# Optimization experiments

Hardware: AMD Instinct MI355X
Metric: run time of the kernel (lower is better)

Reference implementation:

```python
import jax, jax.numpy as jnp
import numpy as np

NUM_KEYPOINTS = 2048
SAMPLE_RADIUS = 1.6
NUM_SECTORS = 6
NEG = jnp.float32(-1e10)
POS = jnp.float32(1e10)


def setup_inputs() -> dict:
    key = jax.random.key(0)
    kxy, kz, kc, kcz, kd, ky = jax.random.split(key, 6)
    B, N, M = 2, 65536, 128
    pts_xy = jax.random.uniform(kxy, (B, N, 2), minval=-70.0, maxval=70.0)
    pts_z = jax.random.uniform(kz, (B, N, 1), minval=-3.0, maxval=1.0)
    points = jnp.concatenate([pts_xy, pts_z], axis=-1)  # [B,N,3]
    ctr_xy = jax.random.uniform(kc, (B, M, 2), minval=-60.0, maxval=60.0)
    ctr_z = jax.random.uniform(kcz, (B, M, 1), minval=-2.0, maxval=0.0)
    dims = jax.random.uniform(kd, (B, M, 3), minval=1.0, maxval=4.5)
    yaw = jax.random.uniform(ky, (B, M, 1), minval=-np.pi, maxval=np.pi)
    rois = jnp.concatenate([ctr_xy, ctr_z, dims, yaw], axis=-1)  # [B,M,7]
    return {"points": points, "rois": rois}


def _masked_fps(xyz, mask, K):
    """Farthest point sampling restricted to mask; returns K indices into xyz.
    Matches mmcv furthest_point_sample: squared distances, start at first point."""
    first = jnp.argmax(mask)  # first valid point in original order
    dmin = jnp.where(mask, POS, NEG)

    def step(carry, _):
        dmin, last = carry
        d = jnp.sum((xyz - xyz[last]) ** 2, axis=-1)
        dmin = jnp.minimum(dmin, jnp.where(mask, d, NEG))
        nxt = jnp.argmax(dmin)
        return (dmin, nxt), nxt

    (_, _), rest = jax.lax.scan(step, (dmin, first), None, length=K - 1)
    return jnp.concatenate([first[None], rest])  # [K]


def _spc_single(points, rois):
    """points: [N,3] float, rois: [M,7]. Returns [NUM_KEYPOINTS,3]."""
    N = points.shape[0]
    K = NUM_KEYPOINTS
    # geometric center: z += dz/2 (done in forward before sampling)
    rois = rois.at[:, 2].add(rois[:, 5] * 0.5)
    # --- sample_points_with_roi: point-to-ROI-center distance filter ---
    diff = points[:, None, :] - rois[None, :, 0:3]          # [N,M,3]
    dist = jnp.linalg.norm(diff, axis=-1)                   # [N,M]
    min_dis = jnp.min(dist, axis=-1)
    min_idx = jnp.argmin(dist, axis=-1)
    roi_max_dim = jnp.linalg.norm(rois[min_idx, 3:6] * 0.5, axis=-1)
    valid = min_dis < roi_max_dim + SAMPLE_RADIUS           # [N]
    total = jnp.maximum(jnp.sum(valid), 1)
    # --- sector_fps ---
    sector_size = 2.0 * np.pi / NUM_SECTORS
    angles = jnp.arctan2(points[:, 1], points[:, 0]) + np.pi
    sector = jnp.clip(jnp.floor(angles / sector_size), 0, NUM_SECTORS).astype(jnp.int32)
    masks = valid[None, :] & (sector[None, :] == jnp.arange(NUM_SECTORS)[:, None])  # [S,N]
    cnt = jnp.sum(masks, axis=-1)                           # [S]
    # per-sector budget: min(cnt_k, ceil(cnt_k / total * K)), 0 for empty sectors
    n_k = jnp.minimum(cnt, jnp.ceil(cnt.astype(jnp.float32) * K / total).astype(cnt.dtype))
    fps_idx = jax.vmap(_masked_fps, in_axes=(None, 0, None))(points, masks, K)  # [S,K]
    # concatenate the first n_k picks of each sector in sector order
    offsets = jnp.concatenate([jnp.zeros((1,), n_k.dtype), jnp.cumsum(n_k)[:-1]])
    pos = offsets[:, None] + jnp.arange(K)[None, :]          # [S,K] slot in concat order
    keep = jnp.arange(K)[None, :] < n_k[:, None]
    pos = jnp.where(keep, pos, K)                            # out-of-range -> dropped
    buf = jnp.zeros((K,), jnp.int32)
    buf = buf.at[pos.reshape(-1)].set(fps_idx.reshape(-1).astype(jnp.int32), mode='drop')
    # truncate / cyclic-repeat to exactly K keypoints
    s_total = jnp.maximum(jnp.sum(n_k), 1)
    out_idx = buf[jnp.arange(K) % s_total]
    return points[out_idx]                                   # [K,3]


def reference(points, rois):
    return jax.vmap(_spc_single)(points, rois)  # [B,K,3]
```

## Files before the change

### kernel.cpp

```cpp
#include <hip/hip_runtime.h>
#include <cmath>
#include <cstdint>

#pragma clang fp contract(off)

#define B_ 2
#define N_ 65536
#define M_ 128
#define K_ 2048
#define S_ 6
#define NBLK 256
#define CT 256
#define FPS_T 512
#define NW 8
#define RMAX 8
#define CAP (FPS_T * RMAX)

#define PI_F 3.14159265358979323846f
#define SS_F 1.0471975511965976f

__device__ __forceinline__ unsigned long long wave_max_u64_dpp(unsigned long long key) {
#define DPP_STEP(CTRL)                                                          \
    {                                                                           \
        unsigned lo = (unsigned)key, hi = (unsigned)(key >> 32);                \
        unsigned olo = (unsigned)__builtin_amdgcn_update_dpp(0, (int)lo, CTRL, 0xf, 0xf, true); \
        unsigned ohi = (unsigned)__builtin_amdgcn_update_dpp(0, (int)hi, CTRL, 0xf, 0xf, true); \
        unsigned long long o = ((unsigned long long)ohi << 32) | olo;           \
        if (o > key) key = o;                                                   \
    }
    DPP_STEP(0x111)
    DPP_STEP(0x112)
    DPP_STEP(0x114)
    DPP_STEP(0x118)
    DPP_STEP(0x142)
    DPP_STEP(0x143)
#undef DPP_STEP
    return key;
}

__global__ __launch_bounds__(CT)
void k_classify(const float* __restrict__ points, const float* __restrict__ rois,
                int* __restrict__ sec_id, int* __restrict__ blkcnt,
                int* __restrict__ done_ctr) {
    __shared__ float4 sroi[M_];
    __shared__ int lc[8];
    int blk = blockIdx.x;
    int gid = blk * CT + threadIdx.x;
    int b = gid >> 16;
    if (blk == 0 && threadIdx.x == 0) *done_ctr = 0;
    if (threadIdx.x < M_) {
        const float* r = rois + ((size_t)b * M_ + threadIdx.x) * 7;
        float cz = r[2] + r[5] * 0.5f;
        float hx = r[3] * 0.5f, hy = r[4] * 0.5f, hz = r[5] * 0.5f;
        sroi[threadIdx.x] = make_float4(r[0], r[1], cz, sqrtf((hx*hx + hy*hy) + hz*hz));
    }
    if (threadIdx.x < 8) lc[threadIdx.x] = 0;
    __syncthreads();

    const float* p = points + (size_t)gid * 3;
    float px = p[0], py = p[1], pz = p[2];
    float best = 1e30f; int bi = 0;
    for (int m = 0; m < M_; m++) {
        float4 c = sroi[m];
        float dx = px - c.x, dy = py - c.y, dz = pz - c.z;
        float d = sqrtf((dx*dx + dy*dy) + dz*dz);
        if (d < best) { best = d; bi = m; }
    }
    bool valid = best < (sroi[bi].w + 1.6f);

    float a = atan2f(py, px) + PI_F;
    float fs = floorf(a / SS_F);
    fs = fminf(fmaxf(fs, 0.0f), 6.0f);
    int sec = (int)fs;

    sec_id[gid] = valid ? sec : -1;
    if (valid) atomicAdd(&lc[sec], 1);
    __syncthreads();
    if (threadIdx.x < 8) blkcnt[blk * 8 + threadIdx.x] = lc[threadIdx.x];
}

__global__ __launch_bounds__(CT)
void k_compact(const float* __restrict__ points, const int* __restrict__ sec_id,
               const int* __restrict__ blkcnt,
               int* __restrict__ cnt, int* __restrict__ offv,
               int* __restrict__ n_needed, int* __restrict__ sec_base_g,
               int* __restrict__ s_total,
               int* __restrict__ comp_idx, float4* __restrict__ comp_xyz) {
    __shared__ int scnt_lds[NBLK][8];
    __shared__ int sbase[6], blkb[6], stot[8];
    __shared__ int lc[4 * 6];
    int blk = blockIdx.x;
    int b = blk >> 8, j = blk & 255;
    int tid = threadIdx.x, lane = tid & 63, wid = tid >> 6;

    {
        const int4* src = (const int4*)(blkcnt + (size_t)(b * NBLK + tid) * 8);
        int4 r0 = src[0], r1 = src[1];
        *(int4*)&scnt_lds[tid][0] = r0;
        *(int4*)&scnt_lds[tid][4] = r1;
    }
    __syncthreads();
    if (tid < 7) {
        int run = 0, pref = 0;
        for (int j2 = 0; j2 < NBLK; j2++) {
            if (j2 == j) pref = run;
            run += scnt_lds[j2][tid];
        }
        stot[tid] = run;
        if (tid < 6) blkb[tid] = pref;
    }
    __syncthreads();
    if (tid == 0) {
        int sb = 0;
        for (int s = 0; s < 6; s++) { sbase[s] = sb; sb += stot[s]; }
    }
    if (j == 0 && tid == 64) {
        int total = 0;
        for (int s = 0; s < 7; s++) total += stot[s];
        if (total < 1) total = 1;
        int sb = 0, snk = 0;
        for (int s = 0; s < 6; s++) {
            int cs = stot[s];
            int nk = (int)ceilf((float)cs * 2048.0f / (float)total);
            if (nk > cs) nk = cs;
            offv[b * 6 + s] = snk;
            int need = 0;
            if (snk < K_) { need = K_ - snk; if (need > nk) need = nk; }
            n_needed[b * 6 + s] = need;
            sec_base_g[b * 6 + s] = sb;
            cnt[b * 8 + s] = cs;
            sb += cs; snk += nk;
        }
        s_total[b] = (snk < 1) ? 1 : snk;
    }

    int gid = blk * CT + tid;
    int sec = sec_id[gid];
    unsigned long long mymask = 0;
    for (int s = 0; s < 6; s++) {
        unsigned long long m = __ballot(sec == s);
        if (sec == s) mymask = m;
        if (lane == 0) lc[wid * 6 + s] = __popcll(m);
    }
    __syncthreads();
    if (sec >= 0 && sec < 6) {
        int woff = 0;
        for (int w = 0; w < wid; w++) woff += lc[w * 6 + sec];
        int rank = __popcll(mymask & ((1ull << lane) - 1ull));
        int addr = b * N_ + sbase[sec] + blkb[sec] + woff + rank;
        const float* p = points + (size_t)gid * 3;
        comp_idx[addr] = gid & (N_ - 1);
        comp_xyz[addr] = make_float4(p[0], p[1], p[2], 0.0f);
    }
}

__global__ __launch_bounds__(FPS_T, 2)
void k_fps(const int* __restrict__ cnt, const int* __restrict__ sec_base,
           const int* __restrict__ offv, const int* __restrict__ n_needed,
           const float4* __restrict__ comp_xyz,
           float* __restrict__ dmin_g, int* __restrict__ buf,
           const float* __restrict__ points, const int* __restrict__ comp_idx,
           const int* __restrict__ s_total, float* __restrict__ out,
           int* __restrict__ done_ctr) {
    __shared__ float4 sxyz[CAP];
    __shared__ int pick_lds[K_];
    __shared__ unsigned long long skey[2][NW];
    __shared__ int is_last;
    int b = blockIdx.x / S_, s = blockIdx.x % S_;
    int need = n_needed[b * 6 + s];
    int cs = cnt[b * 8 + s];
    int base = b * N_ + sec_base[b * 6 + s];
    const float4* cxyz = comp_xyz + base;
    int off = b * K_ + offv[b * 6 + s];
    int tid = threadIdx.x, lane = tid & 63, wid = tid >> 6;

    if (need > 0 && cs <= CAP) {
        float px[RMAX], py[RMAX], pz[RMAX], dmv[RMAX];
        #pragma unroll
        for (int r = 0; r < RMAX; r++) {
            if (r * FPS_T < cs) {
                int i = tid + r * FPS_T;
                if (i < cs) {
                    float4 q = cxyz[i];
                    sxyz[i] = q;
                    px[r] = q.x; py[r] = q.y; pz[r] = q.z;
                    dmv[r] = 1e10f;
                }
            }
        }
        if (tid == 0) pick_lds[0] = 0;
        __syncthreads();
        float4 l4 = sxyz[0];
        float lx = l4.x, ly = l4.y, lz = l4.z;

        #pragma unroll 1
        for (int k = 1; k < need; k++) {
            unsigned long long t[4] = {0ull, 0ull, 0ull, 0ull};
            #pragma unroll
            for (int r = 0; r < RMAX; r++) {
                if (r * FPS_T < cs) {
                    int i = tid + r * FPS_T;
                    if (i < cs) {
                        float dx = px[r] - lx, dy = py[r] - ly, dz = pz[r] - lz;
                        float d = (dx*dx + dy*dy) + dz*dz;
                        float nd = fminf(dmv[r], d);
                        dmv[r] = nd;
                        unsigned long long kk =
                            ((unsigned long long)__float_as_uint(nd) << 32) | (unsigned)(~(unsigned)i);
                        if (kk > t[r & 3]) t[r & 3] = kk;
                    }
                }
            }
            unsigned long long ta = (t[1] > t[0]) ? t[1] : t[0];
            unsigned long long tb = (t[3] > t[2]) ? t[3] : t[2];
            unsigned long long key = (tb > ta) ? tb : ta;
            key = wave_max_u64_dpp(key);
            int par = k & 1;
            if (lane == 63) skey[par][wid] = key;
            __syncthreads();
            unsigned long long q0 = skey[par][0], q1 = skey[par][1];
            unsigned long long q2 = skey[par][2], q3 = skey[par][3];
            unsigned long long q4 = skey[par][4], q5 = skey[par][5];
            unsigned long long q6 = skey[par][6], q7 = skey[par][7];
            q0 = (q1 > q0) ? q1 : q0;
            q2 = (q3 > q2) ? q3 : q2;
            q4 = (q5 > q4) ? q5 : q4;
            q6 = (q7 > q6) ? q7 : q6;
            q0 = (q2 > q0) ? q2 : q0;
            q4 = (q6 > q4) ? q6 : q4;
            unsigned long long bk = (q4 > q0) ? q4 : q0;
            int bix = (int)(~(unsigned)(bk & 0xFFFFFFFFull));
            if (tid == 0) pick_lds[k] = bix;
            float4 n4 = sxyz[bix];
            lx = n4.x; ly = n4.y; lz = n4.z;
        }
        __syncthreads();
        #pragma unroll 1
        for (int i = tid; i < need; i += FPS_T)
            buf[off + i] = base + pick_lds[i];
    } else if (need > 0) {
        float* dm = dmin_g + base;
        if (tid == 0) pick_lds[0] = 0;
        __syncthreads();
        float4 f0 = cxyz[0];
        float lx = f0.x, ly = f0.y, lz = f0.z;
        #pragma unroll 1
        for (int k = 1; k < need; k++) {
            unsigned long long key = 0;
            #pragma unroll 1
            for (int i = tid; i < cs; i += FPS_T) {
                float4 q = cxyz[i];
                float dx = q.x - lx, dy = q.y - ly, dz = q.z - lz;
                float d = (dx*dx + dy*dy) + dz*dz;
                float prev = (k == 1) ? 1e10f : dm[i];
                float nd = fminf(prev, d);
                dm[i] = nd;
                unsigned long long kk =
                    ((unsigned long long)__float_as_uint(nd) << 32) | (unsigned)(~(unsigned)i);
                if (kk > key) key = kk;
            }
            key = wave_max_u64_dpp(key);
            int par = k & 1;
            if (lane == 63) skey[par][wid] = key;
            __syncthreads();
            unsigned long long q0 = skey[par][0], q1 = skey[par][1];
            unsigned long long q2 = skey[par][2], q3 = skey[par][3];
            unsigned long long q4 = skey[par][4], q5 = skey[par][5];
            unsigned long long q6 = skey[par][6], q7 = skey[par][7];
            q0 = (q1 > q0) ? q1 : q0;
            q2 = (q3 > q2) ? q3 : q2;
            q4 = (q5 > q4) ? q5 : q4;
            q6 = (q7 > q6) ? q7 : q6;
            q0 = (q2 > q0) ? q2 : q0;
            q4 = (q6 > q4) ? q6 : q4;
            unsigned long long bk = (q4 > q0) ? q4 : q0;
            int bix = (int)(~(unsigned)(bk & 0xFFFFFFFFull));
            if (tid == 0) pick_lds[k] = bix;
            float4 n4 = cxyz[bix];
            lx = n4.x; ly = n4.y; lz = n4.z;
        }
        __syncthreads();
        #pragma unroll 1
        for (int i = tid; i < need; i += FPS_T)
            buf[off + i] = base + pick_lds[i];
    }

    __syncthreads();
    if (tid == 0) {
        __threadfence();
        int old = atomicAdd(done_ctr, 1);
        is_last = (old == B_ * S_ - 1) ? 1 : 0;
    }
    __syncthreads();
    if (is_last) {
        __threadfence();
        #pragma unroll 1
        for (int i = tid; i < B_ * K_; i += FPS_T) {
            int b2 = i / K_, j2 = i - b2 * K_;
            int st = s_total[b2];
            int g = buf[b2 * K_ + (j2 % st)];
            int idx = comp_idx[g];
            const float* p = points + ((size_t)b2 * N_ + idx) * 3;
            float* o = out + (size_t)i * 3;
            o[0] = p[0]; o[1] = p[1]; o[2] = p[2];
        }
    }
}

extern "C" void kernel_launch(void* const* d_in, const int* in_sizes, int n_in,
                              void* d_out, int out_size, void* d_ws, size_t ws_size,
                              hipStream_t stream) {
    const float* points = (const float*)d_in[0];
    const float* rois   = (const float*)d_in[1];
    float* out = (float*)d_out;

    char* w = (char*)d_ws;
    auto carve = [&](size_t bytes) -> char* {
        char* p = w; w += (bytes + 255) & ~(size_t)255; return p;
    };
    int*    sec_id   = (int*)   carve((size_t)B_ * N_ * sizeof(int));
    int*    blkcnt   = (int*)   carve((size_t)B_ * NBLK * 8 * sizeof(int));
    int*    cnt      = (int*)   carve((size_t)B_ * 8 * sizeof(int));
    int*    offv     = (int*)   carve((size_t)B_ * 6 * sizeof(int));
    int*    n_needed = (int*)   carve((size_t)B_ * 6 * sizeof(int));
    int*    sec_base = (int*)   carve((size_t)B_ * 6 * sizeof(int));
    int*    s_total  = (int*)   carve((size_t)B_ * sizeof(int));
    int*    buf      = (int*)   carve((size_t)B_ * K_ * sizeof(int));
    int*    comp_idx = (int*)   carve((size_t)B_ * N_ * sizeof(int));
    float4* comp_xyz = (float4*)carve((size_t)B_ * N_ * sizeof(float4));
    float*  dmin_g   = (float*) carve((size_t)B_ * N_ * sizeof(float));
    int*    done_ctr = (int*)   carve(sizeof(int));

    hipLaunchKernelGGL(k_classify, dim3(B_ * NBLK), dim3(CT), 0, stream,
                       points, rois, sec_id, blkcnt, done_ctr);
    hipLaunchKernelGGL(k_compact, dim3(B_ * NBLK), dim3(CT), 0, stream,
                       points, sec_id, blkcnt, cnt, offv, n_needed, sec_base,
                       s_total, comp_idx, comp_xyz);
    hipLaunchKernelGGL(k_fps, dim3(B_ * S_), dim3(FPS_T), 0, stream,
                       cnt, sec_base, offv, n_needed, comp_xyz, dmin_g, buf,
                       points, comp_idx, s_total, out, done_ctr);
}
```

Baseline: 397.0 us.

## Fuse classify and compact kernels via cooperative grid sync

Merges the classification and compaction kernels into one cooperative kernel that uses a grid-wide barrier between per-block counting and the scatter phase. Point coordinates and sector ids stay in registers, so the sec_id buffer write/read and the second points load go away, along with one kernel launch. In exchange it needs all 512 blocks co-resident for the cooperative launch, and the grid sync itself costs something.

```diff
diff --git a/kernel.cpp b/kernel.cpp
--- a/kernel.cpp
+++ b/kernel.cpp
@@ -1,8 +1,11 @@
 #include <hip/hip_runtime.h>
+#include <hip/hip_cooperative_groups.h>
 #include <cmath>
 #include <cstdint>
 
 #pragma clang fp contract(off)
+
+namespace cg = cooperative_groups;
 
 #define B_ 2
 #define N_ 65536
@@ -39,22 +42,33 @@
 }
 
 __global__ __launch_bounds__(CT)
-void k_classify(const float* __restrict__ points, const float* __restrict__ rois,
-                int* __restrict__ sec_id, int* __restrict__ blkcnt,
-                int* __restrict__ done_ctr) {
+void k_pre(const float* __restrict__ points, const float* __restrict__ rois,
+           int* __restrict__ blkcnt,
+           int* __restrict__ cnt, int* __restrict__ offv,
+           int* __restrict__ n_needed, int* __restrict__ sec_base_g,
+           int* __restrict__ s_total,
+           int* __restrict__ comp_idx, float4* __restrict__ comp_xyz,
+           int* __restrict__ done_ctr) {
     __shared__ float4 sroi[M_];
-    __shared__ int lc[8];
+    __shared__ int lc8[8];
+    __shared__ int scnt_lds[NBLK][8];
+    __shared__ int sbase[6], blkb[6], stot[8];
+    __shared__ int lc[4 * 6];
+
     int blk = blockIdx.x;
-    int gid = blk * CT + threadIdx.x;
+    int tid = threadIdx.x, lane = tid & 63, wid = tid >> 6;
+    int gid = blk * CT + tid;
     int b = gid >> 16;
-    if (blk == 0 && threadIdx.x == 0) *done_ctr = 0;
-    if (threadIdx.x < M_) {
-        const float* r = rois + ((size_t)b * M_ + threadIdx.x) * 7;
+    int j = blk & 255;
+
+    if (blk == 0 && tid == 0) *done_ctr = 0;
+    if (tid < M_) {
+        const float* r = rois + ((size_t)b * M_ + tid) * 7;
         float cz = r[2] + r[5] * 0.5f;
         float hx = r[3] * 0.5f, hy = r[4] * 0.5f, hz = r[5] * 0.5f;
-        sroi[threadIdx.x] = make_float4(r[0], r[1], cz, sqrtf((hx*hx + hy*hy) + hz*hz));
-    }
-    if (threadIdx.x < 8) lc[threadIdx.x] = 0;
+        sroi[tid] = make_float4(r[0], r[1], cz, sqrtf((hx*hx + hy*hy) + hz*hz));
+    }
+    if (tid < 8) lc8[tid] = 0;
     __syncthreads();
 
     const float* p = points + (size_t)gid * 3;
@@ -71,27 +85,14 @@
     float a = atan2f(py, px) + PI_F;
     float fs = floorf(a / SS_F);
     fs = fminf(fmaxf(fs, 0.0f), 6.0f);
-    int sec = (int)fs;
-
-    sec_id[gid] = valid ? sec : -1;
-    if (valid) atomicAdd(&lc[sec], 1);
-    __syncthreads();
-    if (threadIdx.x < 8) blkcnt[blk * 8 + threadIdx.x] = lc[threadIdx.x];
-}
-
-__global__ __launch_bounds__(CT)
-void k_compact(const float* __restrict__ points, const int* __restrict__ sec_id,
-               const int* __restrict__ blkcnt,
-               int* __restrict__ cnt, int* __restrict__ offv,
-               int* __restrict__ n_needed, int* __restrict__ sec_base_g,
-               int* __restrict__ s_total,
-               int* __restrict__ comp_idx, float4* __restrict__ comp_xyz) {
-    __shared__ int scnt_lds[NBLK][8];
-    __shared__ int sbase[6], blkb[6], stot[8];
-    __shared__ int lc[4 * 6];
-    int blk = blockIdx.x;
-    int b = blk >> 8, j = blk & 255;
-    int tid = threadIdx.x, lane = tid & 63, wid = tid >> 6;
+    int sec = valid ? (int)fs : -1;
+
+    if (valid) atomicAdd(&lc8[(int)fs], 1);
+    __syncthreads();
+    if (tid < 8) blkcnt[blk * 8 + tid] = lc8[tid];
+
+    __threadfence();
+    cg::this_grid().sync();
 
     {
         const int4* src = (const int4*)(blkcnt + (size_t)(b * NBLK + tid) * 8);
@@ -134,8 +135,6 @@
         s_total[b] = (snk < 1) ? 1 : snk;
     }
 
-    int gid = blk * CT + tid;
-    int sec = sec_id[gid];
     unsigned long long mymask = 0;
     for (int s = 0; s < 6; s++) {
         unsigned long long m = __ballot(sec == s);
@@ -148,9 +147,8 @@
         for (int w = 0; w < wid; w++) woff += lc[w * 6 + sec];
         int rank = __popcll(mymask & ((1ull << lane) - 1ull));
         int addr = b * N_ + sbase[sec] + blkb[sec] + woff + rank;
-        const float* p = points + (size_t)gid * 3;
         comp_idx[addr] = gid & (N_ - 1);
-        comp_xyz[addr] = make_float4(p[0], p[1], p[2], 0.0f);
+        comp_xyz[addr] = make_float4(px, py, pz, 0.0f);
     }
 }
 
@@ -318,7 +316,6 @@
     auto carve = [&](size_t bytes) -> char* {
         char* p = w; w += (bytes + 255) & ~(size_t)255; return p;
     };
-    int*    sec_id   = (int*)   carve((size_t)B_ * N_ * sizeof(int));
     int*    blkcnt   = (int*)   carve((size_t)B_ * NBLK * 8 * sizeof(int));
     int*    cnt      = (int*)   carve((size_t)B_ * 8 * sizeof(int));
     int*    offv     = (int*)   carve((size_t)B_ * 6 * sizeof(int));
@@ -331,11 +328,14 @@
     float*  dmin_g   = (float*) carve((size_t)B_ * N_ * sizeof(float));
     int*    done_ctr = (int*)   carve(sizeof(int));
 
-    hipLaunchKernelGGL(k_classify, dim3(B_ * NBLK), dim3(CT), 0, stream,
-                       points, rois, sec_id, blkcnt, done_ctr);
-    hipLaunchKernelGGL(k_compact, dim3(B_ * NBLK), dim3(CT), 0, stream,
-                       points, sec_id, blkcnt, cnt, offv, n_needed, sec_base,
-                       s_total, comp_idx, comp_xyz);
+    {
+        void* args[] = { (void*)&points, (void*)&rois, (void*)&blkcnt,
+                         (void*)&cnt, (void*)&offv, (void*)&n_needed,
+                         (void*)&sec_base, (void*)&s_total,
+                         (void*)&comp_idx, (void*)&comp_xyz, (void*)&done_ctr };
+        hipLaunchCooperativeKernel((const void*)k_pre, dim3(B_ * NBLK), dim3(CT),
+                                   args, 0, stream);
+    }
     hipLaunchKernelGGL(k_fps, dim3(B_ * S_), dim3(FPS_T), 0, stream,
                        cnt, sec_base, offv, n_needed, comp_xyz, dmin_g, buf,
                        points, comp_idx, s_total, out, done_ctr);
```

Result: slower. 466.2 us (+17.4%).
